# Kernel optimization log

Measured on AMD Instinct MI355X. Metric: run time of the kernel, lower is better.

The kernel has to match this reference:

```python
import jax, jax.numpy as jnp
import numpy as np

B, D, H, O = 16384, 256, 64, 256


def setup_inputs() -> dict:
    key = jax.random.key(0)
    ks = jax.random.split(key, 7)
    s1 = 1.0  # Linear(1,H): fan_in=1 -> U(-1,1)
    sH = 1.0 / np.sqrt(H)
    sD = 1.0 / np.sqrt(D)
    return {
        "x": jax.random.normal(ks[0], (B, D), dtype=jnp.float32),
        "W1": jax.random.uniform(ks[1], (D, H), jnp.float32, -s1, s1),
        "b1": jax.random.uniform(ks[2], (D, H), jnp.float32, -s1, s1),
        "W2": jax.random.uniform(ks[3], (D, H), jnp.float32, -sH, sH),
        "b2": jax.random.uniform(ks[4], (D,), jnp.float32, -sH, sH),
        "Wc": jax.random.uniform(ks[5], (O, D), jnp.float32, -sD, sD),
        "bc": jax.random.uniform(ks[6], (O,), jnp.float32, -sD, sD),
    }


def reference(x, W1, b1, W2, b2, Wc, bc):
    # Per-feature tiny MLP, batched over the feature axis D.
    # hidden: [B, D, H]
    h = jax.nn.relu(x[:, :, None] * W1[None, :, :] + b1[None, :, :])
    # collapse hidden -> scalar per feature: [B, D]
    u = jnp.einsum("bdh,dh->bd", h, W2) + b2[None, :]
    # combiner Linear(D, O)
    return u @ Wc.T + bc[None, :]
```

## Files before the change

### kernel.cpp

```cpp
#include <hip/hip_runtime.h>
#include <hip/hip_bf16.h>

#define B_N 16384
#define D_N 256
#define H_N 64
#define O_N 256

typedef __attribute__((ext_vector_type(8))) short short8;
typedef __attribute__((ext_vector_type(4))) float f32x4;

static __device__ __forceinline__ unsigned short f2bf(float f) {
  unsigned int v = __float_as_uint(f);
  unsigned int r = (v + 0x7fffu + ((v >> 16) & 1u)) >> 16;
  return (unsigned short)r;
}

__global__ __launch_bounds__(256, 2) void kan_fused(
    const float* __restrict__ x, const float* __restrict__ W1,
    const float* __restrict__ b1, const float* __restrict__ W2,
    const float* __restrict__ b2, const float* __restrict__ Wc,
    const float* __restrict__ bc, float* __restrict__ out) {
  __shared__ float w1s[64][H_N];
  __shared__ float b1s[64][H_N];
  __shared__ float w2s[64][H_N];
  __shared__ unsigned short uT[32 * 256];

  const int tid = threadIdx.x;
  const int dl  = tid & 63;
  const int wv  = tid >> 6;
  const int b0  = blockIdx.x * 32;

  for (int c = 0; c < 4; ++c) {
    const int d0 = c * 64;
    for (int i = tid; i < 64 * H_N; i += 256) {
      const int dd = i >> 6;
      const int h  = i & 63;
      const int hs = h ^ ((dd & 7) << 2);
      const int g  = (d0 + dd) * H_N + h;
      w1s[dd][hs] = W1[g];
      b1s[dd][hs] = b1[g];
      w2s[dd][hs] = W2[g];
    }
    __syncthreads();

    float xv[8], acc[8];
#pragma unroll
    for (int r = 0; r < 8; ++r) {
      xv[r]  = x[(b0 + wv * 8 + r) * D_N + d0 + dl];
      acc[r] = 0.f;
    }
    const int hswz = (dl & 7) << 2;
#pragma unroll
    for (int h0 = 0; h0 < H_N; h0 += 4) {
      const int hb = h0 ^ hswz;
      const f32x4 a4 = *reinterpret_cast<const f32x4*>(&w1s[dl][hb]);
      const f32x4 c4 = *reinterpret_cast<const f32x4*>(&b1s[dl][hb]);
      const f32x4 w4 = *reinterpret_cast<const f32x4*>(&w2s[dl][hb]);
#pragma unroll
      for (int k = 0; k < 4; ++k) {
#pragma unroll
        for (int r = 0; r < 8; ++r) {
          float t = fmaf(xv[r], a4[k], c4[k]);
          t = fmaxf(t, 0.f);
          acc[r] = fmaf(t, w4[k], acc[r]);
        }
      }
    }
    const float bias = b2[d0 + dl];
#pragma unroll
    for (int r = 0; r < 8; ++r) {
      const int row = wv * 8 + r;
      int byte = row * 512 + (d0 + dl) * 2;
      byte ^= (row & 7) << 4;
      *reinterpret_cast<unsigned short*>(reinterpret_cast<char*>(uT) + byte) =
          f2bf(acc[r] + bias);
    }
    __syncthreads();
  }

  const int n0   = wv * 64;
  const int mrow = dl & 15;
  const int kgrp = dl >> 4;

  f32x4 acc2[2][4];
#pragma unroll
  for (int i = 0; i < 2; ++i)
#pragma unroll
    for (int j = 0; j < 4; ++j) acc2[i][j] = (f32x4)(0.f);

#pragma unroll
  for (int ks = 0; ks < 8; ++ks) {
    const int k0 = ks * 32 + kgrp * 8;
    short8 afrag[2];
#pragma unroll
    for (int i = 0; i < 2; ++i) {
      const int row = i * 16 + mrow;
      int byte = row * 512 + k0 * 2;
      byte ^= (row & 7) << 4;
      afrag[i] = *reinterpret_cast<const short8*>(
          reinterpret_cast<const char*>(uT) + byte);
    }
    short8 bfrag[4];
#pragma unroll
    for (int j = 0; j < 4; ++j) {
      const float* p = Wc + (n0 + j * 16 + mrow) * D_N + k0;
      const f32x4 lo = *reinterpret_cast<const f32x4*>(p);
      const f32x4 hi = *reinterpret_cast<const f32x4*>(p + 4);
      short8 bf;
#pragma unroll
      for (int q = 0; q < 4; ++q) bf[q] = (short)f2bf(lo[q]);
#pragma unroll
      for (int q = 0; q < 4; ++q) bf[q + 4] = (short)f2bf(hi[q]);
      bfrag[j] = bf;
    }
#pragma unroll
    for (int i = 0; i < 2; ++i)
#pragma unroll
      for (int j = 0; j < 4; ++j)
        acc2[i][j] = __builtin_amdgcn_mfma_f32_16x16x32_bf16(
            afrag[i], bfrag[j], acc2[i][j], 0, 0, 0);
  }

#pragma unroll
  for (int j = 0; j < 4; ++j) {
    const int colg = n0 + j * 16 + mrow;
    const float bcv = bc[colg];
#pragma unroll
    for (int i = 0; i < 2; ++i) {
#pragma unroll
      for (int q = 0; q < 4; ++q) {
        const int rowg = b0 + i * 16 + kgrp * 4 + q;
        out[rowg * O_N + colg] = acc2[i][j][q] + bcv;
      }
    }
  }
}

extern "C" void kernel_launch(void* const* d_in, const int* in_sizes, int n_in,
                              void* d_out, int out_size, void* d_ws, size_t ws_size,
                              hipStream_t stream) {
  const float* x  = (const float*)d_in[0];
  const float* W1 = (const float*)d_in[1];
  const float* b1 = (const float*)d_in[2];
  const float* W2 = (const float*)d_in[3];
  const float* b2 = (const float*)d_in[4];
  const float* Wc = (const float*)d_in[5];
  const float* bc = (const float*)d_in[6];
  float* out = (float*)d_out;

  kan_fused<<<dim3(B_N / 32), dim3(256), 0, stream>>>(x, W1, b1, W2, b2, Wc, bc, out);
}
```

Measured before the change: 114.2 us.

## Read MLP weights from global, drop LDS staging, pre-convert Wc to bf16

Removes the per-chunk LDS staging of W1/b1/W2 and its barriers. Each thread now reads its own feature row directly from global memory through cache, which shrinks LDS use so launch bounds can rise to 4 blocks per CU. Adds a small pre-kernel that converts Wc to bf16 in the workspace once per call, so the MFMA stage loads bf16 fragments instead of converting floats. The cost is uncoalesced per-thread row reads of the weights, one extra kernel launch, and possible register pressure at the higher occupancy target.

```diff
diff --git a/kernel.cpp b/kernel.cpp
--- a/kernel.cpp
+++ b/kernel.cpp
@@ -7,6 +7,7 @@
 #define O_N 256
 
 typedef __attribute__((ext_vector_type(8))) short short8;
+typedef __attribute__((ext_vector_type(4))) short short4v;
 typedef __attribute__((ext_vector_type(4))) float f32x4;
 
 static __device__ __forceinline__ unsigned short f2bf(float f) {
@@ -15,14 +16,22 @@
   return (unsigned short)r;
 }
 
-__global__ __launch_bounds__(256, 2) void kan_fused(
+__global__ void wc_prep(const float* __restrict__ Wc, unsigned short* __restrict__ o) {
+  const int i = (blockIdx.x * 256 + threadIdx.x) * 4;
+  const f32x4 v = *reinterpret_cast<const f32x4*>(Wc + i);
+  short4v s;
+#pragma unroll
+  for (int q = 0; q < 4; ++q) s[q] = (short)f2bf(v[q]);
+  *reinterpret_cast<short4v*>(o + i) = s;
+}
+
+template <bool WCB>
+__global__ __launch_bounds__(256, 4) void kan_fused(
     const float* __restrict__ x, const float* __restrict__ W1,
     const float* __restrict__ b1, const float* __restrict__ W2,
     const float* __restrict__ b2, const float* __restrict__ Wc,
-    const float* __restrict__ bc, float* __restrict__ out) {
-  __shared__ float w1s[64][H_N];
-  __shared__ float b1s[64][H_N];
-  __shared__ float w2s[64][H_N];
+    const unsigned short* __restrict__ Wcb, const float* __restrict__ bc,
+    float* __restrict__ out) {
   __shared__ unsigned short uT[32 * 256];
 
   const int tid = threadIdx.x;
@@ -30,32 +39,25 @@
   const int wv  = tid >> 6;
   const int b0  = blockIdx.x * 32;
 
+#pragma unroll
   for (int c = 0; c < 4; ++c) {
-    const int d0 = c * 64;
-    for (int i = tid; i < 64 * H_N; i += 256) {
-      const int dd = i >> 6;
-      const int h  = i & 63;
-      const int hs = h ^ ((dd & 7) << 2);
-      const int g  = (d0 + dd) * H_N + h;
-      w1s[dd][hs] = W1[g];
-      b1s[dd][hs] = b1[g];
-      w2s[dd][hs] = W2[g];
-    }
-    __syncthreads();
+    const int d0   = c * 64;
+    const int drow = d0 + dl;
+    const float* w1p = W1 + drow * H_N;
+    const float* b1p = b1 + drow * H_N;
+    const float* w2p = W2 + drow * H_N;
 
     float xv[8], acc[8];
 #pragma unroll
     for (int r = 0; r < 8; ++r) {
-      xv[r]  = x[(b0 + wv * 8 + r) * D_N + d0 + dl];
+      xv[r]  = x[(b0 + wv * 8 + r) * D_N + drow];
       acc[r] = 0.f;
     }
-    const int hswz = (dl & 7) << 2;
 #pragma unroll
     for (int h0 = 0; h0 < H_N; h0 += 4) {
-      const int hb = h0 ^ hswz;
-      const f32x4 a4 = *reinterpret_cast<const f32x4*>(&w1s[dl][hb]);
-      const f32x4 c4 = *reinterpret_cast<const f32x4*>(&b1s[dl][hb]);
-      const f32x4 w4 = *reinterpret_cast<const f32x4*>(&w2s[dl][hb]);
+      const f32x4 a4 = *reinterpret_cast<const f32x4*>(w1p + h0);
+      const f32x4 c4 = *reinterpret_cast<const f32x4*>(b1p + h0);
+      const f32x4 w4 = *reinterpret_cast<const f32x4*>(w2p + h0);
 #pragma unroll
       for (int k = 0; k < 4; ++k) {
 #pragma unroll
@@ -66,17 +68,17 @@
         }
       }
     }
-    const float bias = b2[d0 + dl];
+    const float bias = b2[drow];
 #pragma unroll
     for (int r = 0; r < 8; ++r) {
       const int row = wv * 8 + r;
-      int byte = row * 512 + (d0 + dl) * 2;
+      int byte = row * 512 + drow * 2;
       byte ^= (row & 7) << 4;
       *reinterpret_cast<unsigned short*>(reinterpret_cast<char*>(uT) + byte) =
           f2bf(acc[r] + bias);
     }
-    __syncthreads();
   }
+  __syncthreads();
 
   const int n0   = wv * 64;
   const int mrow = dl & 15;
@@ -103,15 +105,20 @@
     short8 bfrag[4];
 #pragma unroll
     for (int j = 0; j < 4; ++j) {
-      const float* p = Wc + (n0 + j * 16 + mrow) * D_N + k0;
-      const f32x4 lo = *reinterpret_cast<const f32x4*>(p);
-      const f32x4 hi = *reinterpret_cast<const f32x4*>(p + 4);
-      short8 bf;
+      const int n = n0 + j * 16 + mrow;
+      if (WCB) {
+        bfrag[j] = *reinterpret_cast<const short8*>(Wcb + n * D_N + k0);
+      } else {
+        const float* p = Wc + n * D_N + k0;
+        const f32x4 lo = *reinterpret_cast<const f32x4*>(p);
+        const f32x4 hi = *reinterpret_cast<const f32x4*>(p + 4);
+        short8 bf;
 #pragma unroll
-      for (int q = 0; q < 4; ++q) bf[q] = (short)f2bf(lo[q]);
+        for (int q = 0; q < 4; ++q) bf[q] = (short)f2bf(lo[q]);
 #pragma unroll
-      for (int q = 0; q < 4; ++q) bf[q + 4] = (short)f2bf(hi[q]);
-      bfrag[j] = bf;
+        for (int q = 0; q < 4; ++q) bf[q + 4] = (short)f2bf(hi[q]);
+        bfrag[j] = bf;
+      }
     }
 #pragma unroll
     for (int i = 0; i < 2; ++i)
@@ -148,5 +155,13 @@
   const float* bc = (const float*)d_in[6];
   float* out = (float*)d_out;
 
-  kan_fused<<<dim3(B_N / 32), dim3(256), 0, stream>>>(x, W1, b1, W2, b2, Wc, bc, out);
+  if (ws_size >= (size_t)(O_N * D_N * sizeof(unsigned short))) {
+    unsigned short* Wcb = (unsigned short*)d_ws;
+    wc_prep<<<dim3(O_N * D_N / (256 * 4)), dim3(256), 0, stream>>>(Wc, Wcb);
+    kan_fused<true><<<dim3(B_N / 32), dim3(256), 0, stream>>>(
+        x, W1, b1, W2, b2, Wc, Wcb, bc, out);
+  } else {
+    kan_fused<false><<<dim3(B_N / 32), dim3(256), 0, stream>>>(
+        x, W1, b1, W2, b2, Wc, (const unsigned short*)nullptr, bc, out);
+  }
 }
```

Measured after the change: 132.7 us. +16.1%, slower.
